# Kernel tuning notes

Hardware: AMD Instinct MI355X
Metric: run time of the kernel (lower is better)

Reference implementation:

```python
import jax, jax.numpy as jnp
import numpy as np

N_NODES = 100000
N_EDGES = 1200000
IN_CH = 64
HID = 64


def sage_conv(x, src, dst, Wl, b, Wr, num_nodes):
    # mean aggregation of source-node features at target nodes (flow=source_to_target)
    msg = x[src]                                      # [E, C] gather
    agg = jax.ops.segment_sum(msg, dst, num_segments=num_nodes)  # [N, C]
    cnt = jax.ops.segment_sum(jnp.ones((src.shape[0],), x.dtype), dst,
                              num_segments=num_nodes)
    mean = agg / jnp.maximum(cnt, 1.0)[:, None]
    # PyG SAGEConv: lin_l(aggregated) + bias + lin_r(root)
    return mean @ Wl + b + x @ Wr


def setup_inputs() -> dict:
    key = jax.random.key(0)
    ks = jax.random.split(key, 10)
    x = jax.random.normal(ks[0], (N_NODES, IN_CH), dtype=jnp.float32)
    edge_index = jax.random.randint(ks[1], (2, N_EDGES), 0, N_NODES, dtype=jnp.int64)
    s1 = 1.0 / np.sqrt(IN_CH)
    s2 = 1.0 / np.sqrt(HID)
    W1l = jax.random.uniform(ks[2], (IN_CH, HID), jnp.float32, -s1, s1)
    b1 = jax.random.uniform(ks[3], (HID,), jnp.float32, -s1, s1)
    W1r = jax.random.uniform(ks[4], (IN_CH, HID), jnp.float32, -s1, s1)
    W2l = jax.random.uniform(ks[5], (HID, HID), jnp.float32, -s2, s2)
    b2 = jax.random.uniform(ks[6], (HID,), jnp.float32, -s2, s2)
    W2r = jax.random.uniform(ks[7], (HID, HID), jnp.float32, -s2, s2)
    Wfc = jax.random.uniform(ks[8], (HID, 1), jnp.float32, -s2, s2)
    bfc = jax.random.uniform(ks[9], (1,), jnp.float32, -s2, s2)
    return {"x": x, "edge_index": edge_index, "W1l": W1l, "b1": b1, "W1r": W1r,
            "W2l": W2l, "b2": b2, "W2r": W2r, "Wfc": Wfc, "bfc": bfc}


def reference(x, edge_index, W1l, b1, W1r, W2l, b2, W2r, Wfc, bfc):
    num_nodes = x.shape[0]
    src, dst = edge_index[0], edge_index[1]
    x = jnp.nan_to_num(x, nan=0.0)
    # layer 1: SAGEConv -> ReLU (dropout is identity in eval)
    h = jax.nn.relu(sage_conv(x, src, dst, W1l, b1, W1r, num_nodes))
    # layer 2
    h = jax.nn.relu(sage_conv(h, src, dst, W2l, b2, W2r, num_nodes))
    pred = (h @ Wfc + bfc)[:, 0]  # (num_nodes,)
    return pred
```

## Files before the change

### kernel.cpp

```cpp
#include <hip/hip_runtime.h>

#define NN_NODES 100000
#define NN_EDGES 1200000
#define CH 64
#define BUCKET_NODES 200
#define NBUCKETS (NN_NODES / BUCKET_NODES)
#define EPB 4096
#define PREP_THREADS 1024
#define XCDS 8
#define PCAP 768
#define BMAX (XCDS * PCAP)

#define PA_BLOCKS ((NN_EDGES + EPB - 1) / EPB)
#define CV_ITEMS (NN_NODES * CH / 4)
#define CVB_BLOCKS ((CV_ITEMS + 1023) / 1024)
#define WP_ITEMS (64 * 128)
#define WP_BLOCKS ((WP_ITEMS + PREP_THREADS - 1) / PREP_THREADS)

#define FUSED_NODES 16
#define FUSED_BLOCKS (NN_NODES / FUSED_NODES)

typedef __attribute__((ext_vector_type(8))) short bf16x8;
typedef __attribute__((ext_vector_type(4))) float f32x4;

__device__ __forceinline__ float nan0(float v) { return v == v ? v : 0.0f; }

__device__ __forceinline__ unsigned short f2bf(float f) {
    unsigned u = __float_as_uint(f);
    return (unsigned short)((u + 0x7fffu + ((u >> 16) & 1u)) >> 16);
}

__device__ __forceinline__ unsigned xcc_id() {
    unsigned x;
    asm volatile("s_getreg_b32 %0, hwreg(HW_REG_XCC_ID)" : "=s"(x));
    return x & (XCDS - 1);
}

__global__ __launch_bounds__(PREP_THREADS) void prep_kernel(
    const float* __restrict__ W1l, const float* __restrict__ W1r,
    const float* __restrict__ W2l, const float* __restrict__ W2r,
    unsigned short* __restrict__ Wt1, unsigned short* __restrict__ Wt2,
    const int* __restrict__ src, const int* __restrict__ dst,
    int* __restrict__ bcnt, unsigned int* __restrict__ bbuf)
{
    __shared__ int lhist[NBUCKETS];
    __shared__ int lbase[NBUCKETS];
    int tid = threadIdx.x;
    int bid = blockIdx.x;

    if (bid < PA_BLOCKS) {
        int e0 = bid * EPB;
        unsigned xcc = xcc_id();

        for (int i = tid; i < NBUCKETS; i += PREP_THREADS) lhist[i] = 0;
        __syncthreads();

        int eb = e0 + tid * 4;
        int nv = NN_EDGES - eb;
        if (nv > 4) nv = 4;
        int da[4] = {-1, -1, -1, -1};
        if (nv == 4) {
            int4 dv = *(const int4*)(dst + eb);
            da[0] = dv.x; da[1] = dv.y; da[2] = dv.z; da[3] = dv.w;
        } else {
            for (int r = 0; r < nv; r++) da[r] = dst[eb + r];
        }
        #pragma unroll
        for (int r = 0; r < 4; r++)
            if (da[r] >= 0) atomicAdd(&lhist[da[r] / BUCKET_NODES], 1);
        __syncthreads();

        for (int i = tid; i < NBUCKETS; i += PREP_THREADS) {
            int c = lhist[i];
            lbase[i] = c > 0 ? atomicAdd(&bcnt[i * XCDS + xcc], c) : 0;
            lhist[i] = 0;
        }
        __syncthreads();

        int sa[4] = {0, 0, 0, 0};
        if (nv == 4) {
            int4 sv = *(const int4*)(src + eb);
            sa[0] = sv.x; sa[1] = sv.y; sa[2] = sv.z; sa[3] = sv.w;
        } else {
            for (int r = 0; r < nv; r++) sa[r] = src[eb + r];
        }
        #pragma unroll
        for (int r = 0; r < 4; r++) {
            int d = da[r];
            if (d >= 0) {
                int b = d / BUCKET_NODES;
                int dloc = d - b * BUCKET_NODES;
                int pos = lbase[b] + atomicAdd(&lhist[b], 1);
                if (pos < PCAP)
                    bbuf[((size_t)b * XCDS + xcc) * PCAP + pos] =
                        ((unsigned)dloc << 24) | (unsigned)sa[r];
            }
        }
    } else {
        int i = (bid - PA_BLOCKS) * PREP_THREADS + tid;
        if (i < WP_ITEMS) {
            int n = i >> 7;
            int k = i & 127;
            float v1 = (k < 64) ? W1l[k * 64 + n] : W1r[(k - 64) * 64 + n];
            float v2 = (k < 64) ? W2l[k * 64 + n] : W2r[(k - 64) * 64 + n];
            Wt1[i] = f2bf(v1);
            Wt2[i] = f2bf(v2);
        }
    }
}

__global__ __launch_bounds__(256) void passB_kernel(
    const int* __restrict__ bcnt, const unsigned int* __restrict__ bbuf,
    int* __restrict__ col, int* __restrict__ rowptr,
    const float* __restrict__ x, unsigned short* __restrict__ xb)
{
    __shared__ int hist[BUCKET_NODES];
    __shared__ int cur[BUCKET_NODES];
    __shared__ int sc[256];
    __shared__ unsigned int stage[BMAX];
    int b = blockIdx.x;
    int t = threadIdx.x;

    if (b >= NBUCKETS) {
        int base = (b - NBUCKETS) * 1024 + t;
        #pragma unroll
        for (int k = 0; k < 4; k++) {
            int i = base + k * 256;
            if (i < CV_ITEMS) {
                float4 v = ((const float4*)x)[i];
                v.x = nan0(v.x); v.y = nan0(v.y); v.z = nan0(v.z); v.w = nan0(v.w);
                ushort4 o;
                o.x = f2bf(v.x); o.y = f2bf(v.y); o.z = f2bf(v.z); o.w = f2bf(v.w);
                ((ushort4*)xb)[i] = o;
            }
        }
        return;
    }

    for (int i = t; i < BUCKET_NODES; i += 256) hist[i] = 0;

    int part = 0;
    int lim = b * XCDS;
    for (int i = t; i < lim; i += 256) {
        int c = bcnt[i];
        part += c > PCAP ? PCAP : c;
    }
    sc[t] = part;
    __syncthreads();
    #pragma unroll
    for (int off = 128; off > 0; off >>= 1) {
        if (t < off) sc[t] += sc[t + off];
        __syncthreads();
    }
    int base = sc[0];
    __syncthreads();

    int cnt = 0;
    #pragma unroll
    for (int x8 = 0; x8 < XCDS; x8++) {
        int pc = bcnt[b * XCDS + x8];
        if (pc > PCAP) pc = PCAP;
        const unsigned int* seg = bbuf + ((size_t)b * XCDS + x8) * PCAP;
        for (int k = t; k < pc; k += 256) {
            unsigned v = seg[k];
            stage[cnt + k] = v;
            atomicAdd(&hist[v >> 24], 1);
        }
        cnt += pc;
    }
    __syncthreads();

    int own = (t < BUCKET_NODES) ? hist[t] : 0;
    sc[t] = own;
    __syncthreads();
    for (int off = 1; off < 256; off <<= 1) {
        int v = (t >= off) ? sc[t - off] : 0;
        __syncthreads();
        sc[t] += v;
        __syncthreads();
    }
    if (t < BUCKET_NODES) {
        int excl = sc[t] - own;
        rowptr[b * BUCKET_NODES + t] = base + excl;
        cur[t] = excl;
    }
    if (b == NBUCKETS - 1 && t == 0) rowptr[NN_NODES] = base + cnt;
    __syncthreads();

    for (int k = t; k < cnt; k += 256) {
        unsigned v = stage[k];
        int dloc = (int)(v >> 24);
        int pos = atomicAdd(&cur[dloc], 1);
        col[base + pos] = (int)(v & 0xFFFFFFu);
    }
}

template<int LAYER>
__global__ __launch_bounds__(256) void fused_kernel(
    const unsigned short* __restrict__ feat,
    const int* __restrict__ rowptr, const int* __restrict__ col,
    const unsigned short* __restrict__ Wt,
    const float* __restrict__ bias,
    const float* __restrict__ Wfc, const float* __restrict__ bfc,
    unsigned short* __restrict__ hb_out,
    float* __restrict__ out)
{
    __shared__ unsigned short sA[FUSED_NODES][136];
    __shared__ unsigned short sO[FUSED_NODES][72];
    __shared__ float psum[FUSED_NODES];

    int tid = threadIdx.x;
    int n_base = blockIdx.x * FUSED_NODES;

    int w    = tid >> 6;
    int lane = tid & 63;
    int quad = lane >> 4;
    int colx = lane & 15;

    for (int i = tid; i < FUSED_NODES * 8; i += 256) {
        int node = i >> 3;
        int c = i & 7;
        *(uint4*)&sA[node][64 + c * 8] =
            *(const uint4*)(feat + (size_t)(n_base + node) * CH + c * 8);
    }
    if (LAYER == 2 && tid < FUSED_NODES) psum[tid] = 0.f;

    int r0a[4], r1a[4];
    #pragma unroll
    for (int j = 0; j < 4; j++) {
        int node = n_base + w * 4 + j;
        r0a[j] = rowptr[node];
        r1a[j] = rowptr[node + 1];
    }

    int sidx[4][4];
    #pragma unroll
    for (int j = 0; j < 4; j++) {
        int r1 = r1a[j];
        int bi = r0a[j] + quad;
        #pragma unroll
        for (int m = 0; m < 4; m++) {
            int idx = bi + 4 * m;
            sidx[j][m] = col[idx < r1 ? idx : 0];
        }
    }

    uint2 u[4][4];
    #pragma unroll
    for (int j = 0; j < 4; j++) {
        #pragma unroll
        for (int m = 0; m < 4; m++) {
            u[j][m] = *(const uint2*)(feat + (size_t)sidx[j][m] * CH + colx * 4);
        }
    }

    #pragma unroll
    for (int j = 0; j < 4; j++) {
        int nl = w * 4 + j;
        int r0 = r0a[j], r1 = r1a[j];
        float a0[4] = {0, 0, 0, 0};
        #pragma unroll
        for (int m = 0; m < 4; m++) {
            if (r0 + quad + 4 * m < r1) {
                a0[0] += __uint_as_float(u[j][m].x << 16);
                a0[1] += __uint_as_float(u[j][m].x & 0xffff0000u);
                a0[2] += __uint_as_float(u[j][m].y << 16);
                a0[3] += __uint_as_float(u[j][m].y & 0xffff0000u);
            }
        }
        int i = r0 + quad + 16;
        if (i < r1) {
            float b0[4] = {0, 0, 0, 0}, b1[4] = {0, 0, 0, 0};
            for (; i + 4 < r1; i += 8) {
                int s0 = col[i];
                int s1 = col[i + 4];
                uint2 v0 = *(const uint2*)(feat + (size_t)s0 * CH + colx * 4);
                uint2 v1 = *(const uint2*)(feat + (size_t)s1 * CH + colx * 4);
                b0[0] += __uint_as_float(v0.x << 16);
                b0[1] += __uint_as_float(v0.x & 0xffff0000u);
                b0[2] += __uint_as_float(v0.y << 16);
                b0[3] += __uint_as_float(v0.y & 0xffff0000u);
                b1[0] += __uint_as_float(v1.x << 16);
                b1[1] += __uint_as_float(v1.x & 0xffff0000u);
                b1[2] += __uint_as_float(v1.y << 16);
                b1[3] += __uint_as_float(v1.y & 0xffff0000u);
            }
            if (i < r1) {
                int s0 = col[i];
                uint2 v0 = *(const uint2*)(feat + (size_t)s0 * CH + colx * 4);
                b0[0] += __uint_as_float(v0.x << 16);
                b0[1] += __uint_as_float(v0.x & 0xffff0000u);
                b0[2] += __uint_as_float(v0.y << 16);
                b0[3] += __uint_as_float(v0.y & 0xffff0000u);
            }
            #pragma unroll
            for (int q = 0; q < 4; q++) a0[q] += b0[q] + b1[q];
        }
        #pragma unroll
        for (int q = 0; q < 4; q++) {
            a0[q] += __shfl_xor(a0[q], 16, 64);
            a0[q] += __shfl_xor(a0[q], 32, 64);
        }
        if (lane < 16) {
            int deg = r1 - r0;
            float inv = 1.0f / (float)(deg > 0 ? deg : 1);
            ushort4 o;
            o.x = f2bf(a0[0] * inv); o.y = f2bf(a0[1] * inv);
            o.z = f2bf(a0[2] * inv); o.w = f2bf(a0[3] * inv);
            *(ushort4*)&sA[nl][colx * 4] = o;
        }
    }
    __syncthreads();

    const unsigned short* wrow = Wt + (size_t)(w * 16 + colx) * 128;
    float bv = bias[w * 16 + colx];

    f32x4 acc = (f32x4){0.f, 0.f, 0.f, 0.f};
    #pragma unroll
    for (int ks = 0; ks < 4; ks++) {
        bf16x8 bfr = *(const bf16x8*)(wrow + ks * 32 + quad * 8);
        bf16x8 af = *(const bf16x8*)&sA[colx][ks * 32 + quad * 8];
        acc = __builtin_amdgcn_mfma_f32_16x16x32_bf16(af, bfr, acc, 0, 0, 0);
    }

    if (LAYER == 1) {
        #pragma unroll
        for (int r = 0; r < 4; r++) {
            float v = acc[r] + bv;
            v = v > 0.f ? v : 0.f;
            sO[quad * 4 + r][w * 16 + colx] = f2bf(v);
        }
        __syncthreads();
        for (int i = tid; i < FUSED_NODES * 8; i += 256) {
            int node = i >> 3;
            int c = i & 7;
            *(uint4*)(hb_out + (size_t)(n_base + node) * CH + c * 8) =
                *(const uint4*)&sO[node][c * 8];
        }
    } else {
        float wf = Wfc[w * 16 + colx];
        #pragma unroll
        for (int r = 0; r < 4; r++) {
            float v = acc[r] + bv;
            v = v > 0.f ? v : 0.f;
            float p = v * wf;
            p += __shfl_xor(p, 1, 64);
            p += __shfl_xor(p, 2, 64);
            p += __shfl_xor(p, 4, 64);
            p += __shfl_xor(p, 8, 64);
            if (colx == 0) atomicAdd(&psum[quad * 4 + r], p);
        }
        __syncthreads();
        if (tid < FUSED_NODES) out[n_base + tid] = psum[tid] + bfc[0];
    }
}

extern "C" void kernel_launch(void* const* d_in, const int* in_sizes, int n_in,
                              void* d_out, int out_size, void* d_ws, size_t ws_size,
                              hipStream_t stream) {
    const float* x    = (const float*)d_in[0];
    const int*   ei   = (const int*)d_in[1];
    const float* W1l  = (const float*)d_in[2];
    const float* b1   = (const float*)d_in[3];
    const float* W1r  = (const float*)d_in[4];
    const float* W2l  = (const float*)d_in[5];
    const float* b2   = (const float*)d_in[6];
    const float* W2r  = (const float*)d_in[7];
    const float* Wfc  = (const float*)d_in[8];
    const float* bfc  = (const float*)d_in[9];
    float* out = (float*)d_out;

    const int N = NN_NODES;
    const int E = NN_EDGES;
    const int* src = ei;
    const int* dst = ei + E;

    char* ws = (char*)d_ws;
    unsigned short* xb  = (unsigned short*)ws;  ws += (size_t)N * CH * sizeof(unsigned short);
    unsigned short* h1b = (unsigned short*)ws;  ws += (size_t)N * CH * sizeof(unsigned short);
    unsigned short* Wt1 = (unsigned short*)ws;  ws += 64 * 128 * sizeof(unsigned short);
    unsigned short* Wt2 = (unsigned short*)ws;  ws += 64 * 128 * sizeof(unsigned short);
    int* bcnt   = (int*)ws;                     ws += (size_t)NBUCKETS * XCDS * sizeof(int);
    int* rowptr = (int*)ws;                     ws += (size_t)(N + 1) * sizeof(int);
    int* col    = (int*)ws;                     ws += (size_t)E * sizeof(int);
    unsigned int* bbuf = (unsigned int*)ws;     ws += (size_t)NBUCKETS * XCDS * PCAP * sizeof(unsigned int);

    hipMemsetAsync(bcnt, 0, (size_t)NBUCKETS * XCDS * sizeof(int), stream);

    prep_kernel<<<PA_BLOCKS + WP_BLOCKS, PREP_THREADS, 0, stream>>>(
        W1l, W1r, W2l, W2r, Wt1, Wt2, src, dst, bcnt, bbuf);
    passB_kernel<<<NBUCKETS + CVB_BLOCKS, 256, 0, stream>>>(
        bcnt, bbuf, col, rowptr, x, xb);

    fused_kernel<1><<<FUSED_BLOCKS, 256, 0, stream>>>(
        xb, rowptr, col, Wt1, b1, nullptr, nullptr, h1b, nullptr);
    fused_kernel<2><<<FUSED_BLOCKS, 256, 0, stream>>>(
        h1b, rowptr, col, Wt2, b2, Wfc, bfc, nullptr, out);
}
```

Baseline: 194.2 us.

## Add padded per-node first-16 neighbor table to break rowptr→col load chain

While building the CSR, passB now also writes up to the first 16 source indices of each node into a fixed-stride padded array (colp). The fused aggregation kernels read those indices with one vectorized int4 load per node, issued in parallel with the rowptr loads. This removes the dependent rowptr→col→feature load chain for the common low-degree case. The cost is an extra 6.4 MB of scattered writes in passB and extra index reads in each layer, and the per-quad assignment of edges is remapped to match the padded layout.

```diff
diff --git a/kernel.cpp b/kernel.cpp
--- a/kernel.cpp
+++ b/kernel.cpp
@@ -112,10 +112,12 @@
 __global__ __launch_bounds__(256) void passB_kernel(
     const int* __restrict__ bcnt, const unsigned int* __restrict__ bbuf,
     int* __restrict__ col, int* __restrict__ rowptr,
+    int* __restrict__ colp,
     const float* __restrict__ x, unsigned short* __restrict__ xb)
 {
     __shared__ int hist[BUCKET_NODES];
     __shared__ int cur[BUCKET_NODES];
+    __shared__ int start[BUCKET_NODES];
     __shared__ int sc[256];
     __shared__ unsigned int stage[BMAX];
     int b = blockIdx.x;
@@ -183,6 +185,7 @@
         int excl = sc[t] - own;
         rowptr[b * BUCKET_NODES + t] = base + excl;
         cur[t] = excl;
+        start[t] = excl;
     }
     if (b == NBUCKETS - 1 && t == 0) rowptr[NN_NODES] = base + cnt;
     __syncthreads();
@@ -190,8 +193,12 @@
     for (int k = t; k < cnt; k += 256) {
         unsigned v = stage[k];
         int dloc = (int)(v >> 24);
+        int srcv = (int)(v & 0xFFFFFFu);
         int pos = atomicAdd(&cur[dloc], 1);
-        col[base + pos] = (int)(v & 0xFFFFFFu);
+        col[base + pos] = srcv;
+        int slot = pos - start[dloc];
+        if (slot < 16)
+            colp[(b * BUCKET_NODES + dloc) * 16 + slot] = srcv;
     }
 }
 
@@ -199,6 +206,7 @@
 __global__ __launch_bounds__(256) void fused_kernel(
     const unsigned short* __restrict__ feat,
     const int* __restrict__ rowptr, const int* __restrict__ col,
+    const int* __restrict__ colp,
     const unsigned short* __restrict__ Wt,
     const float* __restrict__ bias,
     const float* __restrict__ Wfc, const float* __restrict__ bfc,
@@ -217,6 +225,19 @@
     int quad = lane >> 4;
     int colx = lane & 15;
 
+    int4 cp[4];
+    #pragma unroll
+    for (int j = 0; j < 4; j++) {
+        int node = n_base + w * 4 + j;
+        cp[j] = *(const int4*)&colp[node * 16 + quad * 4];
+    }
+    int r0a[4], r1a[4];
+    #pragma unroll
+    for (int j = 0; j < 4; j++) {
+        int node = n_base + w * 4 + j;
+        r0a[j] = rowptr[node];
+        r1a[j] = rowptr[node + 1];
+    }
     for (int i = tid; i < FUSED_NODES * 8; i += 256) {
         int node = i >> 3;
         int c = i & 7;
@@ -225,24 +246,14 @@
     }
     if (LAYER == 2 && tid < FUSED_NODES) psum[tid] = 0.f;
 
-    int r0a[4], r1a[4];
+    int sidx[4][4];
     #pragma unroll
     for (int j = 0; j < 4; j++) {
-        int node = n_base + w * 4 + j;
-        r0a[j] = rowptr[node];
-        r1a[j] = rowptr[node + 1];
-    }
-
-    int sidx[4][4];
-    #pragma unroll
-    for (int j = 0; j < 4; j++) {
-        int r1 = r1a[j];
-        int bi = r0a[j] + quad;
-        #pragma unroll
-        for (int m = 0; m < 4; m++) {
-            int idx = bi + 4 * m;
-            sidx[j][m] = col[idx < r1 ? idx : 0];
-        }
+        int deg = r1a[j] - r0a[j];
+        sidx[j][0] = (quad * 4 + 0 < deg) ? cp[j].x : 0;
+        sidx[j][1] = (quad * 4 + 1 < deg) ? cp[j].y : 0;
+        sidx[j][2] = (quad * 4 + 2 < deg) ? cp[j].z : 0;
+        sidx[j][3] = (quad * 4 + 3 < deg) ? cp[j].w : 0;
     }
 
     uint2 u[4][4];
@@ -258,10 +269,11 @@
     for (int j = 0; j < 4; j++) {
         int nl = w * 4 + j;
         int r0 = r0a[j], r1 = r1a[j];
+        int deg = r1 - r0;
         float a0[4] = {0, 0, 0, 0};
         #pragma unroll
         for (int m = 0; m < 4; m++) {
-            if (r0 + quad + 4 * m < r1) {
+            if (quad * 4 + m < deg) {
                 a0[0] += __uint_as_float(u[j][m].x << 16);
                 a0[1] += __uint_as_float(u[j][m].x & 0xffff0000u);
                 a0[2] += __uint_as_float(u[j][m].y << 16);
@@ -302,7 +314,6 @@
             a0[q] += __shfl_xor(a0[q], 32, 64);
         }
         if (lane < 16) {
-            int deg = r1 - r0;
             float inv = 1.0f / (float)(deg > 0 ? deg : 1);
             ushort4 o;
             o.x = f2bf(a0[0] * inv); o.y = f2bf(a0[1] * inv);
@@ -383,6 +394,7 @@
     int* bcnt   = (int*)ws;                     ws += (size_t)NBUCKETS * XCDS * sizeof(int);
     int* rowptr = (int*)ws;                     ws += (size_t)(N + 1) * sizeof(int);
     int* col    = (int*)ws;                     ws += (size_t)E * sizeof(int);
+    int* colp   = (int*)ws;                     ws += (size_t)N * 16 * sizeof(int);
     unsigned int* bbuf = (unsigned int*)ws;     ws += (size_t)NBUCKETS * XCDS * PCAP * sizeof(unsigned int);
 
     hipMemsetAsync(bcnt, 0, (size_t)NBUCKETS * XCDS * sizeof(int), stream);
@@ -390,10 +402,10 @@
     prep_kernel<<<PA_BLOCKS + WP_BLOCKS, PREP_THREADS, 0, stream>>>(
         W1l, W1r, W2l, W2r, Wt1, Wt2, src, dst, bcnt, bbuf);
     passB_kernel<<<NBUCKETS + CVB_BLOCKS, 256, 0, stream>>>(
-        bcnt, bbuf, col, rowptr, x, xb);
+        bcnt, bbuf, col, rowptr, colp, x, xb);
 
     fused_kernel<1><<<FUSED_BLOCKS, 256, 0, stream>>>(
-        xb, rowptr, col, Wt1, b1, nullptr, nullptr, h1b, nullptr);
+        xb, rowptr, col, colp, Wt1, b1, nullptr, nullptr, h1b, nullptr);
     fused_kernel<2><<<FUSED_BLOCKS, 256, 0, stream>>>(
-        h1b, rowptr, col, Wt2, b2, Wfc, bfc, nullptr, out);
-}
+        h1b, rowptr, col, colp, Wt2, b2, Wfc, bfc, nullptr, out);
+}
```

After: 190.3 us. -2.0%, faster.
